# Optimization experiments

Hardware: AMD Instinct MI355X
Metric: run time of the kernel (lower is better)

## Reference

```python
import jax, jax.numpy as jnp
import numpy as np

D_K = 128
SCALER = np.sqrt(D_K).astype(np.float32)

def setup_inputs() -> dict:
    key = jax.random.key(0)
    kq, kk, kv = jax.random.split(key, 3)
    B, L, D = 16, 2048, D_K
    q = jax.random.normal(kq, (B, L, D), dtype=jnp.float32)
    k = jax.random.normal(kk, (B, L, D), dtype=jnp.float32)
    v = jax.random.normal(kv, (B, L, D), dtype=jnp.float32)
    return {"q": q, "k": k, "v": v}

def reference(q, k, v):
    # score[b, i, j] = q[b, i, :] . k[b, j, :] / sqrt(d_k)
    score = jnp.einsum('bid,bjd->bij', q, k) / SCALER
    attn = jax.nn.softmax(score, axis=-1)
    # output[b, i, :] = sum_j attn[b, i, j] * v[b, j, :]
    return jnp.einsum('bij,bjd->bid', attn, v)
```

## Files before the change

### kernel.cpp

```cpp
#include <hip/hip_runtime.h>
#include <stdint.h>


typedef short bf16x8 __attribute__((ext_vector_type(8)));
typedef float f32x4 __attribute__((ext_vector_type(4)));
typedef unsigned int u32;
typedef unsigned short u16;

#define L_SEQ  2048
#define D_HEAD 128
#define TSZ    8388608u
#define W_PART (2u * TSZ)
#define W_LSUM (W_PART + 768u * 32768u)
#define WS_NEED (W_LSUM + 768u * 128u * 4u)

__device__ __forceinline__ unsigned pk2(float lo, float hi) {
    union { float f; unsigned u; } a, b;
    a.f = lo; b.f = hi;
    return __builtin_amdgcn_perm(b.u + 0x8000u, a.u + 0x8000u, 0x07060302u);
}
__device__ __forceinline__ float ex2(float x) { return __builtin_amdgcn_exp2f(x); }
__device__ __forceinline__ float bflo(unsigned w) {
    union { unsigned u; float f; } v; v.u = w << 16; return v.f;
}
__device__ __forceinline__ float bfhi(unsigned w) {
    union { unsigned u; float f; } v; v.u = w & 0xffff0000u; return v.f;
}
__device__ __forceinline__ void gl_lds16(const u16* g, u16* l) {
    __builtin_amdgcn_global_load_lds(
        (const __attribute__((address_space(1))) u32*)g,
        (__attribute__((address_space(3))) u32*)l, 16, 0, 0);
}

__global__ __launch_bounds__(256, 4)
void prepass(const float* __restrict__ K, const float* __restrict__ V,
             u16* __restrict__ kb, u16* __restrict__ vt) {
    const int id = blockIdx.x, t = threadIdx.x;
    if (id < 512) {
        const float* src = K + (size_t)id * 64 * 128;
        u16*        dst = kb + (size_t)id * 64 * 128;
        const int r = t >> 2;
        #pragma unroll
        for (int i = 0; i < 4; ++i) {
            int gp = (t & 3) * 4 + i;
            int gs = gp ^ (r & 7);
            const float* s = src + r * 128 + gs * 8;
            float4 x0 = *(const float4*)s, x1 = *(const float4*)(s + 4);
            uint4 w;
            w.x = pk2(x0.x, x0.y); w.y = pk2(x0.z, x0.w);
            w.z = pk2(x1.x, x1.y); w.w = pk2(x1.z, x1.w);
            *(uint4*)(dst + r * 128 + gp * 8) = w;
        }
    } else {
        __shared__ __align__(16) u16 vl[128 * 72];
        const int bid = id - 512;
        const float* src = V + (size_t)bid * 64 * 128;
        const int vcc = t & 31, vgk = t >> 5;
        union { float4 v; float f[4]; } vr[8];
        const float* vp = src + (size_t)(vgk * 8) * 128 + vcc * 4;
        #pragma unroll
        for (int r = 0; r < 8; ++r) vr[r].v = *(const float4*)(vp + (size_t)r * 128);
        #pragma unroll
        for (int dd = 0; dd < 4; ++dd) {
            uint4 w;
            w.x = pk2(vr[0].f[dd], vr[1].f[dd]);
            w.y = pk2(vr[2].f[dd], vr[3].f[dd]);
            w.z = pk2(vr[4].f[dd], vr[5].f[dd]);
            w.w = pk2(vr[6].f[dd], vr[7].f[dd]);
            *(uint4*)(&vl[(vcc * 4 + dd) * 72 + vgk * 8]) = w;
        }
        __syncthreads();
        u16* dst = vt + (size_t)bid * 8192;
        #pragma unroll
        for (int i = 0; i < 4; ++i) {
            int flat = t + 256 * i;
            int d = flat >> 3, gp = flat & 7;
            uint4 w = *(const uint4*)(&vl[d * 72 + ((gp ^ (d & 7)) * 8)]);
            *(uint4*)(dst + (size_t)flat * 8) = w;
        }
    }
}

__global__ __launch_bounds__(256, 2)
void attn3(const float* __restrict__ Qg, const u16* __restrict__ kb,
           const u16* __restrict__ vt, u16* __restrict__ part,
           float* __restrict__ lsum) {
    __shared__ __align__(16) char smem[49152];
    const int tid = threadIdx.x;
    const int wv = tid >> 6, lane = tid & 63;
    const int c = lane & 15, qd = lane >> 4, cx = c & 7;
    const int bid = blockIdx.x;
    const int p = bid & 255, kvh = bid >> 8;
    const int b = p & 15, qblk = p >> 4;
    const int t0 = kvh * 11;
    const int nt = (kvh < 2) ? 11 : 10;

    const float* Qp = Qg + (size_t)b * L_SEQ * D_HEAD;
    const u16*   Kp = kb + (size_t)b * L_SEQ * D_HEAD + (size_t)t0 * 8192;
    const u16*   Vp = vt + (size_t)b * 32 * 8192 + (size_t)t0 * 8192;
    u16* Kl = (u16*)smem;
    u16* Vl = (u16*)(smem + 16384);
    u16* Pl = (u16*)(smem + 32768) + wv * 2048;

    const int so = wv * 2048 + lane * 8;
    const int psw = (c & 7) << 1;

    #pragma unroll
    for (int i = 0; i < 4; ++i) {
        gl_lds16(Kp + so + i * 512, Kl + so + i * 512);
        gl_lds16(Vp + so + i * 512, Vl + so + i * 512);
    }

    const float QS = 1.4426950408889634f / 11.313708498984761f;
    bf16x8 qf[2][4];
    #pragma unroll
    for (int s = 0; s < 2; ++s) {
        const float* qrow = Qp + (size_t)(qblk * 128 + wv * 32 + s * 16 + c) * 128 + qd * 8;
        #pragma unroll
        for (int kt = 0; kt < 4; ++kt) {
            float4 x0 = *(const float4*)(qrow + kt * 32);
            float4 x1 = *(const float4*)(qrow + kt * 32 + 4);
            union { unsigned u[4]; bf16x8 v; } tt;
            tt.u[0] = pk2(x0.x * QS, x0.y * QS);
            tt.u[1] = pk2(x0.z * QS, x0.w * QS);
            tt.u[2] = pk2(x1.x * QS, x1.y * QS);
            tt.u[3] = pk2(x1.z * QS, x1.w * QS);
            qf[s][kt] = tt.v;
        }
    }

    f32x4 acc[2][8];
    #pragma unroll
    for (int s = 0; s < 2; ++s)
        #pragma unroll
        for (int dt = 0; dt < 8; ++dt) acc[s][dt] = (f32x4){0.f, 0.f, 0.f, 0.f};
    float lrun[2] = {0.f, 0.f};

    __syncthreads();

    for (int it = 0; it < nt; ++it) {
        f32x4 st[4][2];
        #pragma unroll
        for (int v = 0; v < 4; ++v) {
            st[v][0] = (f32x4){0.f, 0.f, 0.f, 0.f};
            st[v][1] = (f32x4){0.f, 0.f, 0.f, 0.f};
        }
        #pragma unroll
        for (int kt = 0; kt < 4; ++kt) {
            const int g = ((kt * 4 + qd) ^ cx) * 8;
            #pragma unroll
            for (int v = 0; v < 4; ++v) {
                bf16x8 a = *(const bf16x8*)(Kl + (v * 16 + c) * 128 + g);
                st[v][0] = __builtin_amdgcn_mfma_f32_16x16x32_bf16(a, qf[0][kt], st[v][0], 0, 0, 0);
                st[v][1] = __builtin_amdgcn_mfma_f32_16x16x32_bf16(a, qf[1][kt], st[v][1], 0, 0, 0);
            }
        }
        __syncthreads();

        if (it + 1 < nt) {
            const u16* kg = Kp + (size_t)(it + 1) * 8192 + so;
            #pragma unroll
            for (int i = 0; i < 4; ++i) gl_lds16(kg + i * 512, Kl + so + i * 512);
        }

        #pragma unroll
        for (int s = 0; s < 2; ++s) {
            float lsm = 0.f;
            #pragma unroll
            for (int v = 0; v < 4; ++v) {
                float p0 = ex2(st[v][s].x), p1 = ex2(st[v][s].y);
                float p2 = ex2(st[v][s].z), p3 = ex2(st[v][s].w);
                lsm += (p0 + p1) + (p2 + p3);
                uint2 w; w.x = pk2(p0, p1); w.y = pk2(p2, p3);
                int gsw = (v * 4 + qd) ^ psw;
                *(uint2*)(Pl + (s * 16 + c) * 64 + gsw * 4) = w;
            }
            lrun[s] += lsm;
        }
        bf16x8 pf[2][2];
        #pragma unroll
        for (int h = 0; h < 2; ++h) {
            int gsw = (h * 8 + qd * 2) ^ psw;
            #pragma unroll
            for (int s = 0; s < 2; ++s)
                pf[h][s] = *(const bf16x8*)(Pl + (s * 16 + c) * 64 + gsw * 4);
        }

        #pragma unroll
        for (int dt = 0; dt < 8; ++dt) {
            #pragma unroll
            for (int h = 0; h < 2; ++h) {
                bf16x8 a = *(const bf16x8*)(Vl + (dt * 16 + c) * 64 + ((h * 4 + qd) ^ cx) * 8);
                acc[0][dt] = __builtin_amdgcn_mfma_f32_16x16x32_bf16(a, pf[h][0], acc[0][dt], 0, 0, 0);
                acc[1][dt] = __builtin_amdgcn_mfma_f32_16x16x32_bf16(a, pf[h][1], acc[1][dt], 0, 0, 0);
            }
        }
        __syncthreads();

        if (it + 1 < nt) {
            const u16* vg = Vp + (size_t)(it + 1) * 8192 + so;
            #pragma unroll
            for (int i = 0; i < 4; ++i) gl_lds16(vg + i * 512, Vl + so + i * 512);
        }
    }

    float ls[2];
    #pragma unroll
    for (int s = 0; s < 2; ++s) {
        float l = lrun[s];
        l += __shfl_xor(l, 16);
        l += __shfl_xor(l, 32);
        ls[s] = l;
    }
    u16* pb = part + (size_t)bid * 16384;
    #pragma unroll
    for (int s = 0; s < 2; ++s)
        #pragma unroll
        for (int dt = 0; dt < 8; ++dt) {
            f32x4 o = acc[s][dt];
            uint2 w; w.x = pk2(o.x, o.y); w.y = pk2(o.z, o.w);
            *(uint2*)(pb + ((((wv * 2 + s) * 8 + dt) * 64 + lane) << 2)) = w;
        }
    if (qd == 0) {
        lsum[kvh * 32768 + p * 128 + wv * 32 + c]      = ls[0];
        lsum[kvh * 32768 + p * 128 + wv * 32 + 16 + c] = ls[1];
    }
}

__global__ __launch_bounds__(256, 2)
void combine3(const u16* __restrict__ part, const float* __restrict__ lsum,
              float* __restrict__ Og) {
    __shared__ float inv[128];
    __shared__ __align__(16) float Ol[64 * 132];
    const int t = threadIdx.x, p = blockIdx.x;
    const int b = p & 15, qblk = p >> 4;
    if (t < 128) {
        float l0 = lsum[p * 128 + t];
        float l1 = lsum[32768 + p * 128 + t];
        float l2 = lsum[65536 + p * 128 + t];
        inv[t] = 1.0f / (l0 + l1 + l2);
    }
    const uint2* P0 = (const uint2*)(part + (size_t)p * 16384);
    const uint2* P1 = (const uint2*)(part + (size_t)(256 + p) * 16384);
    const uint2* P2 = (const uint2*)(part + (size_t)(512 + p) * 16384);
    __syncthreads();
    #pragma unroll
    for (int h = 0; h < 2; ++h) {
        #pragma unroll
        for (int i = 0; i < 8; ++i) {
            int slot = i * 256 + t;
            int lc = slot >> 6, lane = slot & 63;
            int gc = h * 32 + lc;
            int s = (lc >> 3) & 1, dt = lc & 7;
            int qd = lane >> 4, c = lane & 15;
            int row = (lc >> 4) * 32 + s * 16 + c;
            int d0 = dt * 16 + qd * 4;
            size_t idx = (size_t)gc * 64 + lane;
            uint2 w0 = P0[idx], w1 = P1[idx], w2 = P2[idx];
            float iv = inv[h * 64 + row];
            float4 o;
            o.x = (bflo(w0.x) + bflo(w1.x) + bflo(w2.x)) * iv;
            o.y = (bfhi(w0.x) + bfhi(w1.x) + bfhi(w2.x)) * iv;
            o.z = (bflo(w0.y) + bflo(w1.y) + bflo(w2.y)) * iv;
            o.w = (bfhi(w0.y) + bfhi(w1.y) + bfhi(w2.y)) * iv;
            *(float4*)(&Ol[row * 132 + d0]) = o;
        }
        __syncthreads();
        #pragma unroll
        for (int i = 0; i < 8; ++i) {
            int slot = i * 256 + t;
            int row = slot >> 5, c4 = slot & 31;
            float4 val = *(const float4*)(&Ol[row * 132 + c4 * 4]);
            size_t q = (size_t)b * L_SEQ + qblk * 128 + h * 64 + row;
            *(float4*)(Og + q * D_HEAD + c4 * 4) = val;
        }
        __syncthreads();
    }
}

extern "C" void kernel_launch(void* const* d_in, const int* in_sizes, int n_in,
                              void* d_out, int out_size, void* d_ws, size_t ws_size,
                              hipStream_t stream) {
    const float* q = (const float*)d_in[0];
    const float* k = (const float*)d_in[1];
    const float* v = (const float*)d_in[2];
    float* out = (float*)d_out;
    u16* kb = (u16*)d_ws;
    u16* vt = (u16*)((char*)d_ws + TSZ);
    u16* part = (u16*)((char*)d_ws + W_PART);
    float* ls = (float*)((char*)d_ws + W_LSUM);
    prepass<<<dim3(1024), dim3(256), 0, stream>>>(k, v, kb, vt);
    attn3<<<dim3(768), dim3(256), 0, stream>>>(q, kb, vt, part, ls);
    combine3<<<dim3(256), dim3(256), 0, stream>>>(part, ls, out);
}
```

Before: 139.9 us.

## Double query rows per block and split KV into four equal chunks

Each block now processes 256 query rows (64 per wave) instead of 128, so every K/V tile loaded into LDS is reused across twice as many MFMA operations. The KV split changes from three uneven chunks (11/11/10 tiles) to four equal chunks of 8 tiles, giving 512 blocks and a four-way combine. QK scores are now computed per key subtile and immediately exponentiated and stored to P, which shortens the live range of the score registers. The cost is twice the accumulator registers (acc[4][8]), a larger LDS footprint of 64KB that may limit occupancy at two blocks per CU, and more partial traffic in the combine.

```diff
diff --git a/kernel.cpp b/kernel.cpp
--- a/kernel.cpp
+++ b/kernel.cpp
@@ -11,8 +11,8 @@
 #define D_HEAD 128
 #define TSZ    8388608u
 #define W_PART (2u * TSZ)
-#define W_LSUM (W_PART + 768u * 32768u)
-#define WS_NEED (W_LSUM + 768u * 128u * 4u)
+#define W_LSUM (W_PART + 512u * 65536u)
+#define WS_NEED (W_LSUM + 512u * 256u * 4u)
 
 __device__ __forceinline__ unsigned pk2(float lo, float hi) {
     union { float f; unsigned u; } a, b;
@@ -82,28 +82,26 @@
 }
 
 __global__ __launch_bounds__(256, 2)
-void attn3(const float* __restrict__ Qg, const u16* __restrict__ kb,
+void attn4(const float* __restrict__ Qg, const u16* __restrict__ kb,
            const u16* __restrict__ vt, u16* __restrict__ part,
            float* __restrict__ lsum) {
-    __shared__ __align__(16) char smem[49152];
+    __shared__ __align__(16) char smem[65536];
     const int tid = threadIdx.x;
     const int wv = tid >> 6, lane = tid & 63;
     const int c = lane & 15, qd = lane >> 4, cx = c & 7;
     const int bid = blockIdx.x;
-    const int p = bid & 255, kvh = bid >> 8;
+    const int p = bid & 127, kvh = bid >> 7;
     const int b = p & 15, qblk = p >> 4;
-    const int t0 = kvh * 11;
-    const int nt = (kvh < 2) ? 11 : 10;
 
     const float* Qp = Qg + (size_t)b * L_SEQ * D_HEAD;
-    const u16*   Kp = kb + (size_t)b * L_SEQ * D_HEAD + (size_t)t0 * 8192;
-    const u16*   Vp = vt + (size_t)b * 32 * 8192 + (size_t)t0 * 8192;
+    const u16*   Kp = kb + (size_t)b * L_SEQ * D_HEAD + (size_t)kvh * 8 * 8192;
+    const u16*   Vp = vt + (size_t)b * 32 * 8192 + (size_t)kvh * 8 * 8192;
     u16* Kl = (u16*)smem;
     u16* Vl = (u16*)(smem + 16384);
-    u16* Pl = (u16*)(smem + 32768) + wv * 2048;
+    u16* Pl = (u16*)(smem + 32768) + wv * 4096;
 
     const int so = wv * 2048 + lane * 8;
-    const int psw = (c & 7) << 1;
+    const int psw = cx << 1;
 
     #pragma unroll
     for (int i = 0; i < 4; ++i) {
@@ -112,10 +110,10 @@
     }
 
     const float QS = 1.4426950408889634f / 11.313708498984761f;
-    bf16x8 qf[2][4];
-    #pragma unroll
-    for (int s = 0; s < 2; ++s) {
-        const float* qrow = Qp + (size_t)(qblk * 128 + wv * 32 + s * 16 + c) * 128 + qd * 8;
+    bf16x8 qf[4][4];
+    #pragma unroll
+    for (int s = 0; s < 4; ++s) {
+        const float* qrow = Qp + (size_t)(qblk * 256 + wv * 64 + s * 16 + c) * 128 + qd * 8;
         #pragma unroll
         for (int kt = 0; kt < 4; ++kt) {
             float4 x0 = *(const float4*)(qrow + kt * 32);
@@ -129,140 +127,141 @@
         }
     }
 
-    f32x4 acc[2][8];
-    #pragma unroll
-    for (int s = 0; s < 2; ++s)
+    f32x4 acc[4][8];
+    #pragma unroll
+    for (int s = 0; s < 4; ++s)
         #pragma unroll
         for (int dt = 0; dt < 8; ++dt) acc[s][dt] = (f32x4){0.f, 0.f, 0.f, 0.f};
-    float lrun[2] = {0.f, 0.f};
+    float lrun[4] = {0.f, 0.f, 0.f, 0.f};
 
     __syncthreads();
 
-    for (int it = 0; it < nt; ++it) {
-        f32x4 st[4][2];
+    for (int it = 0; it < 8; ++it) {
         #pragma unroll
         for (int v = 0; v < 4; ++v) {
-            st[v][0] = (f32x4){0.f, 0.f, 0.f, 0.f};
-            st[v][1] = (f32x4){0.f, 0.f, 0.f, 0.f};
-        }
-        #pragma unroll
-        for (int kt = 0; kt < 4; ++kt) {
-            const int g = ((kt * 4 + qd) ^ cx) * 8;
-            #pragma unroll
-            for (int v = 0; v < 4; ++v) {
-                bf16x8 a = *(const bf16x8*)(Kl + (v * 16 + c) * 128 + g);
-                st[v][0] = __builtin_amdgcn_mfma_f32_16x16x32_bf16(a, qf[0][kt], st[v][0], 0, 0, 0);
-                st[v][1] = __builtin_amdgcn_mfma_f32_16x16x32_bf16(a, qf[1][kt], st[v][1], 0, 0, 0);
-            }
-        }
-        __syncthreads();
-
-        if (it + 1 < nt) {
+            bf16x8 a0, a1, a2, a3;
+            {
+                const u16* kr = Kl + (v * 16 + c) * 128;
+                a0 = *(const bf16x8*)(kr + ((0 * 4 + qd) ^ cx) * 8);
+                a1 = *(const bf16x8*)(kr + ((1 * 4 + qd) ^ cx) * 8);
+                a2 = *(const bf16x8*)(kr + ((2 * 4 + qd) ^ cx) * 8);
+                a3 = *(const bf16x8*)(kr + ((3 * 4 + qd) ^ cx) * 8);
+            }
+            f32x4 st[4];
+            #pragma unroll
+            for (int s = 0; s < 4; ++s) {
+                f32x4 z = (f32x4){0.f, 0.f, 0.f, 0.f};
+                z = __builtin_amdgcn_mfma_f32_16x16x32_bf16(a0, qf[s][0], z, 0, 0, 0);
+                z = __builtin_amdgcn_mfma_f32_16x16x32_bf16(a1, qf[s][1], z, 0, 0, 0);
+                z = __builtin_amdgcn_mfma_f32_16x16x32_bf16(a2, qf[s][2], z, 0, 0, 0);
+                z = __builtin_amdgcn_mfma_f32_16x16x32_bf16(a3, qf[s][3], z, 0, 0, 0);
+                st[s] = z;
+            }
+            const int gsw = ((v * 4 + qd) ^ psw) * 4;
+            #pragma unroll
+            for (int s = 0; s < 4; ++s) {
+                float p0 = ex2(st[s].x), p1 = ex2(st[s].y);
+                float p2 = ex2(st[s].z), p3 = ex2(st[s].w);
+                lrun[s] += (p0 + p1) + (p2 + p3);
+                uint2 w; w.x = pk2(p0, p1); w.y = pk2(p2, p3);
+                *(uint2*)(Pl + (s * 16 + c) * 64 + gsw) = w;
+            }
+        }
+        __syncthreads();
+
+        if (it + 1 < 8) {
             const u16* kg = Kp + (size_t)(it + 1) * 8192 + so;
             #pragma unroll
             for (int i = 0; i < 4; ++i) gl_lds16(kg + i * 512, Kl + so + i * 512);
         }
 
         #pragma unroll
-        for (int s = 0; s < 2; ++s) {
-            float lsm = 0.f;
-            #pragma unroll
-            for (int v = 0; v < 4; ++v) {
-                float p0 = ex2(st[v][s].x), p1 = ex2(st[v][s].y);
-                float p2 = ex2(st[v][s].z), p3 = ex2(st[v][s].w);
-                lsm += (p0 + p1) + (p2 + p3);
-                uint2 w; w.x = pk2(p0, p1); w.y = pk2(p2, p3);
-                int gsw = (v * 4 + qd) ^ psw;
-                *(uint2*)(Pl + (s * 16 + c) * 64 + gsw * 4) = w;
-            }
-            lrun[s] += lsm;
-        }
-        bf16x8 pf[2][2];
-        #pragma unroll
         for (int h = 0; h < 2; ++h) {
-            int gsw = (h * 8 + qd * 2) ^ psw;
-            #pragma unroll
-            for (int s = 0; s < 2; ++s)
-                pf[h][s] = *(const bf16x8*)(Pl + (s * 16 + c) * 64 + gsw * 4);
-        }
-
-        #pragma unroll
-        for (int dt = 0; dt < 8; ++dt) {
-            #pragma unroll
-            for (int h = 0; h < 2; ++h) {
+            bf16x8 pf[4];
+            const int gsw = ((h * 8 + qd * 2) ^ psw) * 4;
+            #pragma unroll
+            for (int s = 0; s < 4; ++s)
+                pf[s] = *(const bf16x8*)(Pl + (s * 16 + c) * 64 + gsw);
+            #pragma unroll
+            for (int dt = 0; dt < 8; ++dt) {
                 bf16x8 a = *(const bf16x8*)(Vl + (dt * 16 + c) * 64 + ((h * 4 + qd) ^ cx) * 8);
-                acc[0][dt] = __builtin_amdgcn_mfma_f32_16x16x32_bf16(a, pf[h][0], acc[0][dt], 0, 0, 0);
-                acc[1][dt] = __builtin_amdgcn_mfma_f32_16x16x32_bf16(a, pf[h][1], acc[1][dt], 0, 0, 0);
-            }
-        }
-        __syncthreads();
-
-        if (it + 1 < nt) {
+                acc[0][dt] = __builtin_amdgcn_mfma_f32_16x16x32_bf16(a, pf[0], acc[0][dt], 0, 0, 0);
+                acc[1][dt] = __builtin_amdgcn_mfma_f32_16x16x32_bf16(a, pf[1], acc[1][dt], 0, 0, 0);
+                acc[2][dt] = __builtin_amdgcn_mfma_f32_16x16x32_bf16(a, pf[2], acc[2][dt], 0, 0, 0);
+                acc[3][dt] = __builtin_amdgcn_mfma_f32_16x16x32_bf16(a, pf[3], acc[3][dt], 0, 0, 0);
+            }
+        }
+        __syncthreads();
+
+        if (it + 1 < 8) {
             const u16* vg = Vp + (size_t)(it + 1) * 8192 + so;
             #pragma unroll
             for (int i = 0; i < 4; ++i) gl_lds16(vg + i * 512, Vl + so + i * 512);
         }
     }
 
-    float ls[2];
-    #pragma unroll
-    for (int s = 0; s < 2; ++s) {
+    float ls[4];
+    #pragma unroll
+    for (int s = 0; s < 4; ++s) {
         float l = lrun[s];
         l += __shfl_xor(l, 16);
         l += __shfl_xor(l, 32);
         ls[s] = l;
     }
-    u16* pb = part + (size_t)bid * 16384;
-    #pragma unroll
-    for (int s = 0; s < 2; ++s)
+    u16* pb = part + (size_t)bid * 32768;
+    #pragma unroll
+    for (int s = 0; s < 4; ++s)
         #pragma unroll
         for (int dt = 0; dt < 8; ++dt) {
             f32x4 o = acc[s][dt];
             uint2 w; w.x = pk2(o.x, o.y); w.y = pk2(o.z, o.w);
-            *(uint2*)(pb + ((((wv * 2 + s) * 8 + dt) * 64 + lane) << 2)) = w;
+            int ch = (wv * 4 + s) * 8 + dt;
+            *(uint2*)(pb + (((size_t)ch * 64 + lane) << 2)) = w;
         }
     if (qd == 0) {
-        lsum[kvh * 32768 + p * 128 + wv * 32 + c]      = ls[0];
-        lsum[kvh * 32768 + p * 128 + wv * 32 + 16 + c] = ls[1];
+        float* lp = lsum + (size_t)bid * 256;
+        #pragma unroll
+        for (int s = 0; s < 4; ++s) lp[wv * 64 + s * 16 + c] = ls[s];
     }
 }
 
 __global__ __launch_bounds__(256, 2)
-void combine3(const u16* __restrict__ part, const float* __restrict__ lsum,
+void combine4(const u16* __restrict__ part, const float* __restrict__ lsum,
               float* __restrict__ Og) {
-    __shared__ float inv[128];
+    __shared__ float inv[256];
     __shared__ __align__(16) float Ol[64 * 132];
     const int t = threadIdx.x, p = blockIdx.x;
     const int b = p & 15, qblk = p >> 4;
-    if (t < 128) {
-        float l0 = lsum[p * 128 + t];
-        float l1 = lsum[32768 + p * 128 + t];
-        float l2 = lsum[65536 + p * 128 + t];
-        inv[t] = 1.0f / (l0 + l1 + l2);
-    }
-    const uint2* P0 = (const uint2*)(part + (size_t)p * 16384);
-    const uint2* P1 = (const uint2*)(part + (size_t)(256 + p) * 16384);
-    const uint2* P2 = (const uint2*)(part + (size_t)(512 + p) * 16384);
+    {
+        float l = 0.f;
+        #pragma unroll
+        for (int k = 0; k < 4; ++k) l += lsum[(size_t)(k * 128 + p) * 256 + t];
+        inv[t] = 1.0f / l;
+    }
+    const uint2* P0 = (const uint2*)(part + (size_t)(0 * 128 + p) * 32768);
+    const uint2* P1 = (const uint2*)(part + (size_t)(1 * 128 + p) * 32768);
+    const uint2* P2 = (const uint2*)(part + (size_t)(2 * 128 + p) * 32768);
+    const uint2* P3 = (const uint2*)(part + (size_t)(3 * 128 + p) * 32768);
     __syncthreads();
     #pragma unroll
-    for (int h = 0; h < 2; ++h) {
+    for (int h = 0; h < 4; ++h) {
         #pragma unroll
         for (int i = 0; i < 8; ++i) {
             int slot = i * 256 + t;
             int lc = slot >> 6, lane = slot & 63;
-            int gc = h * 32 + lc;
-            int s = (lc >> 3) & 1, dt = lc & 7;
+            int ch = h * 32 + lc;
+            int s = lc >> 3, dt = lc & 7;
             int qd = lane >> 4, c = lane & 15;
-            int row = (lc >> 4) * 32 + s * 16 + c;
+            int row = s * 16 + c;
             int d0 = dt * 16 + qd * 4;
-            size_t idx = (size_t)gc * 64 + lane;
-            uint2 w0 = P0[idx], w1 = P1[idx], w2 = P2[idx];
+            size_t idx = (size_t)ch * 64 + lane;
+            uint2 w0 = P0[idx], w1 = P1[idx], w2 = P2[idx], w3 = P3[idx];
             float iv = inv[h * 64 + row];
             float4 o;
-            o.x = (bflo(w0.x) + bflo(w1.x) + bflo(w2.x)) * iv;
-            o.y = (bfhi(w0.x) + bfhi(w1.x) + bfhi(w2.x)) * iv;
-            o.z = (bflo(w0.y) + bflo(w1.y) + bflo(w2.y)) * iv;
-            o.w = (bfhi(w0.y) + bfhi(w1.y) + bfhi(w2.y)) * iv;
+            o.x = (bflo(w0.x) + bflo(w1.x) + bflo(w2.x) + bflo(w3.x)) * iv;
+            o.y = (bfhi(w0.x) + bfhi(w1.x) + bfhi(w2.x) + bfhi(w3.x)) * iv;
+            o.z = (bflo(w0.y) + bflo(w1.y) + bflo(w2.y) + bflo(w3.y)) * iv;
+            o.w = (bfhi(w0.y) + bfhi(w1.y) + bfhi(w2.y) + bfhi(w3.y)) * iv;
             *(float4*)(&Ol[row * 132 + d0]) = o;
         }
         __syncthreads();
@@ -271,7 +270,7 @@
             int slot = i * 256 + t;
             int row = slot >> 5, c4 = slot & 31;
             float4 val = *(const float4*)(&Ol[row * 132 + c4 * 4]);
-            size_t q = (size_t)b * L_SEQ + qblk * 128 + h * 64 + row;
+            size_t q = (size_t)b * L_SEQ + qblk * 256 + h * 64 + row;
             *(float4*)(Og + q * D_HEAD + c4 * 4) = val;
         }
         __syncthreads();
@@ -290,6 +289,6 @@
     u16* part = (u16*)((char*)d_ws + W_PART);
     float* ls = (float*)((char*)d_ws + W_LSUM);
     prepass<<<dim3(1024), dim3(256), 0, stream>>>(k, v, kb, vt);
-    attn3<<<dim3(768), dim3(256), 0, stream>>>(q, kb, vt, part, ls);
-    combine3<<<dim3(256), dim3(256), 0, stream>>>(part, ls, out);
-}
+    attn4<<<dim3(512), dim3(256), 0, stream>>>(q, kb, vt, part, ls);
+    combine4<<<dim3(128), dim3(256), 0, stream>>>(part, ls, out);
+}
```

Result: slower. 210.8 us (+50.7%).
